# Kernel optimization log

Measured on AMD Instinct MI355X. Metric: run time of the kernel, lower is better.

Reference implementation:

```python
import jax, jax.numpy as jnp
import numpy as np

N_ITER = 2


def _ssn_iter(pixel_features, sh, sw, n_iter=N_ITER):
    """Faithful JAX port of ssn_iter: returns dense abs_affinity (B, ns, N).

    dist[b,k,p] = ||pix[b,:,p] - spix[b,:,cand_k(p)]||^2 over the 3x3 superpixel
    neighborhood of each pixel's initial label; invalid candidates get +inf
    (softmax -> 0), matching the CUDA PairwiseDistFunction + mask semantics.
    """
    B, C, H, W = pixel_features.shape
    nsh, nsw = H // sh, W // sw
    ns = nsh * nsw
    N = H * W

    # calc_init_centroid: adaptive_avg_pool2d == block mean when divisible
    spix = pixel_features.reshape(B, C, nsh, sh, nsw, sw).mean(axis=(3, 5)).reshape(B, C, ns)

    # init_label_map via nearest interpolation == (row//sh)*nsw + col//sw
    r0 = jnp.repeat(jnp.arange(H) // sh, W)            # (N,) superpixel row of each pixel
    c0 = jnp.tile(jnp.arange(W) // sw, H)              # (N,) superpixel col

    # 9 candidate offsets, ordered as [r-nsw, r, r+nsw] with r in [-1,0,1]
    dr = jnp.repeat(jnp.arange(-1, 2), 3)              # (9,)
    dc = jnp.tile(jnp.arange(-1, 2), 3)                # (9,)
    rr = r0[None, :] + dr[:, None]                     # (9, N)
    cc = c0[None, :] + dc[:, None]                     # (9, N)
    valid = (rr >= 0) & (rr < nsh) & (cc >= 0) & (cc < nsw)   # (9, N)
    sidx = jnp.clip(rr * nsw + cc, 0, ns - 1)          # (9, N) candidate superpixel ids
    pidx = jnp.broadcast_to(jnp.arange(N), (9, N))     # (9, N) pixel ids

    pf = pixel_features.reshape(B, C, N)

    def scatter_dense(a):  # a: (9, N) affinity -> dense (ns, N)
        return jnp.zeros((ns, N), a.dtype).at[sidx, pidx].add(a)

    abs_aff = None
    for k in range(n_iter):
        g = spix[:, :, sidx.reshape(-1)].reshape(B, C, 9, N)          # gather candidates
        d = ((pf[:, :, None, :] - g) ** 2).sum(axis=1)                # (B, 9, N)
        d = jnp.where(valid[None], d, jnp.inf)
        aff = jax.nn.softmax(-d, axis=1)                              # invalid -> 0
        aff = jnp.where(valid[None], aff, 0.0)
        abs_aff = jax.vmap(scatter_dense)(aff)                        # (B, ns, N)
        if k < n_iter - 1:
            num = jnp.einsum('bsn,bcn->bsc', abs_aff, pf)             # dense bmm
            den = abs_aff.sum(axis=2)[..., None] + 1e-16
            spix = (num / den).transpose(0, 2, 1)                     # (B, C, ns)
    return abs_aff


def setup_inputs() -> dict:
    key = jax.random.key(0)
    x = jax.random.normal(key, (2, 64, 320, 320), dtype=jnp.float32)
    return {"pixel_features": x, "stoken_h": 16, "stoken_w": 16}


def reference(pixel_features, stoken_h, stoken_w):
    return _ssn_iter(pixel_features, stoken_h, stoken_w, N_ITER)
```

## Files before the change

### kernel.cpp

```cpp
#include <hip/hip_runtime.h>

#define KB   2
#define KC   64
#define KH   320
#define KW   320
#define KSH  16
#define KSW  16
#define KNSH 20
#define KNSW 20
#define KNS  400
#define KN   102400

typedef float float4v __attribute__((ext_vector_type(4)));

__global__ __launch_bounds__(320) void block_mean_kernel(
    const float* __restrict__ pf, float* __restrict__ spix) {
  int wg = blockIdx.x;
  int rb = wg % KNSH;
  int c  = (wg / KNSH) % KC;
  int b  = wg / (KNSH * KC);
  int t  = threadIdx.x;

  const float* row0 = pf + ((size_t)(b * KC + c) * KH + rb * KSH) * KW;
  float acc = 0.f;
#pragma unroll
  for (int i = 0; i < KSH; ++i) acc += row0[i * KW + t];

#pragma unroll
  for (int off = 8; off > 0; off >>= 1) acc += __shfl_down(acc, off, 16);

  if ((t & 15) == 0)
    spix[(b * KC + c) * KNS + rb * KNSW + (t >> 4)] = acc * (1.0f / (KSH * KSW));
}

__global__ __launch_bounds__(256) void dist_partial_kernel(
    const float* __restrict__ pf, const float* __restrict__ spix,
    float* __restrict__ part, float* __restrict__ den) {
  __shared__ float scand[9][KC];
  __shared__ __align__(16) float aff_s[9][256];
  __shared__ float part_s[9][64];
  __shared__ float den_s[9];

  int wg = blockIdx.x;
  int s  = wg % KNS;
  int b  = wg / KNS;
  int sr = s / KNSW, sc = s % KNSW;
  int t  = threadIdx.x;

  for (int idx = t; idx < 9 * KC; idx += 256) {
    int k = idx >> 6, c = idx & 63;
    int rr = sr + k / 3 - 1, cc = sc + k % 3 - 1;
    float v = 0.f;
    if (rr >= 0 && rr < KNSH && cc >= 0 && cc < KNSW)
      v = spix[(b * KC + c) * KNS + rr * KNSW + cc];
    scand[k][c] = v;
  }
  __syncthreads();

  int ti = t >> 4, tj = t & 15;
  int p = (sr * KSH + ti) * KW + sc * KSW + tj;
  const float* pfp = pf + (size_t)b * KC * KN + p;

  float d[9];
#pragma unroll
  for (int k = 0; k < 9; ++k) d[k] = 0.f;
  for (int c = 0; c < KC; ++c) {
    float x = pfp[(size_t)c * KN];
#pragma unroll
    for (int k = 0; k < 9; ++k) {
      float df = x - scand[k][c];
      d[k] = fmaf(df, df, d[k]);
    }
  }
  float m = 3.4e38f;
#pragma unroll
  for (int k = 0; k < 9; ++k) {
    int rr = sr + k / 3 - 1, cc = sc + k % 3 - 1;
    if (rr >= 0 && rr < KNSH && cc >= 0 && cc < KNSW) m = fminf(m, d[k]);
  }
  float e[9];
  float sum = 0.f;
#pragma unroll
  for (int k = 0; k < 9; ++k) {
    int rr = sr + k / 3 - 1, cc = sc + k % 3 - 1;
    bool valid = (rr >= 0 && rr < KNSH && cc >= 0 && cc < KNSW);
    e[k] = valid ? __expf(m - d[k]) : 0.f;
    sum += e[k];
  }
  float inv = 1.0f / sum;
#pragma unroll
  for (int k = 0; k < 9; ++k) aff_s[k][t] = e[k] * inv;
  __syncthreads();

  int w = t >> 6, l = t & 63;
  int li = l >> 2, lj4 = (l & 3) * 4;
  const float* pfb = pf + ((size_t)b * KC + w * 16) * KN
                   + (sr * KSH + li) * KW + sc * KSW + lj4;

  const float4v a0 = *(const float4v*)(&aff_s[0][l * 4]);
  const float4v a1 = *(const float4v*)(&aff_s[1][l * 4]);
  const float4v a2 = *(const float4v*)(&aff_s[2][l * 4]);
  const float4v a3 = *(const float4v*)(&aff_s[3][l * 4]);
  const float4v a4 = *(const float4v*)(&aff_s[4][l * 4]);
  const float4v a5 = *(const float4v*)(&aff_s[5][l * 4]);
  const float4v a6 = *(const float4v*)(&aff_s[6][l * 4]);
  const float4v a7 = *(const float4v*)(&aff_s[7][l * 4]);
  const float4v a8 = *(const float4v*)(&aff_s[8][l * 4]);

  if (w == 0) {
#define DENK(k, av)                                                       \
    {                                                                     \
      float dv = (av.x + av.y) + (av.z + av.w);                           \
      _Pragma("unroll")                                                   \
      for (int off = 32; off > 0; off >>= 1) dv += __shfl_xor(dv, off, 64); \
      if (l == 0) den_s[k] = dv;                                          \
    }
    DENK(0, a0) DENK(1, a1) DENK(2, a2) DENK(3, a3) DENK(4, a4)
    DENK(5, a5) DENK(6, a6) DENK(7, a7) DENK(8, a8)
#undef DENK
  }

#pragma unroll
  for (int cb = 0; cb < 4; ++cb) {
    float4v x0 = *(const float4v*)(pfb + (size_t)(cb * 4 + 0) * KN);
    float4v x1 = *(const float4v*)(pfb + (size_t)(cb * 4 + 1) * KN);
    float4v x2 = *(const float4v*)(pfb + (size_t)(cb * 4 + 2) * KN);
    float4v x3 = *(const float4v*)(pfb + (size_t)(cb * 4 + 3) * KN);

    float acc[4][9];
#define DOTS(c, xv)                                                        \
    acc[c][0] = fmaf(xv.x, a0.x, fmaf(xv.y, a0.y, fmaf(xv.z, a0.z, xv.w * a0.w))); \
    acc[c][1] = fmaf(xv.x, a1.x, fmaf(xv.y, a1.y, fmaf(xv.z, a1.z, xv.w * a1.w))); \
    acc[c][2] = fmaf(xv.x, a2.x, fmaf(xv.y, a2.y, fmaf(xv.z, a2.z, xv.w * a2.w))); \
    acc[c][3] = fmaf(xv.x, a3.x, fmaf(xv.y, a3.y, fmaf(xv.z, a3.z, xv.w * a3.w))); \
    acc[c][4] = fmaf(xv.x, a4.x, fmaf(xv.y, a4.y, fmaf(xv.z, a4.z, xv.w * a4.w))); \
    acc[c][5] = fmaf(xv.x, a5.x, fmaf(xv.y, a5.y, fmaf(xv.z, a5.z, xv.w * a5.w))); \
    acc[c][6] = fmaf(xv.x, a6.x, fmaf(xv.y, a6.y, fmaf(xv.z, a6.z, xv.w * a6.w))); \
    acc[c][7] = fmaf(xv.x, a7.x, fmaf(xv.y, a7.y, fmaf(xv.z, a7.z, xv.w * a7.w))); \
    acc[c][8] = fmaf(xv.x, a8.x, fmaf(xv.y, a8.y, fmaf(xv.z, a8.z, xv.w * a8.w)));
    DOTS(0, x0) DOTS(1, x1) DOTS(2, x2) DOTS(3, x3)
#undef DOTS

#pragma unroll
    for (int off = 32; off > 0; off >>= 1)
#pragma unroll
      for (int c = 0; c < 4; ++c)
#pragma unroll
        for (int k = 0; k < 9; ++k)
          acc[c][k] += __shfl_xor(acc[c][k], off, 64);

    if (l == 0) {
#pragma unroll
      for (int c = 0; c < 4; ++c)
#pragma unroll
        for (int k = 0; k < 9; ++k)
          part_s[k][w * 16 + cb * 4 + c] = acc[c][k];
    }
  }
  __syncthreads();

  size_t base = ((size_t)b * KNS + s) * 9;
  for (int idx = t; idx < 9 * 64; idx += 256)
    part[base * 64 + idx] = part_s[idx >> 6][idx & 63];
  if (t < 9) den[base + t] = den_s[t];
}

__global__ __launch_bounds__(256) void dist_aff2_kernel(
    const float* __restrict__ pf, const float* __restrict__ part,
    const float* __restrict__ den, float* __restrict__ aff) {
  __shared__ float scand[9][KC];

  int wg = blockIdx.x;
  int s  = wg % KNS;
  int b  = wg / KNS;
  int sr = s / KNSW, sc = s % KNSW;
  int t  = threadIdx.x;

  for (int idx = t; idx < 9 * KC; idx += 256) {
    int k = idx >> 6, c = idx & 63;
    int nr = sr + k / 3 - 1, nc = sc + k % 3 - 1;
    float v = 0.f;
    if (nr >= 0 && nr < KNSH && nc >= 0 && nc < KNSW) {
      float num = 0.f, dsum = 0.f;
#pragma unroll
      for (int j = 0; j < 9; ++j) {
        int rr = nr + j / 3 - 1, cc = nc + j % 3 - 1;
        if (rr >= 0 && rr < KNSH && cc >= 0 && cc < KNSW) {
          size_t base = ((size_t)b * KNS + rr * KNSW + cc) * 9 + (8 - j);
          num  += part[base * 64 + c];
          dsum += den[base];
        }
      }
      v = num / (dsum + 1e-16f);
    }
    scand[k][c] = v;
  }
  __syncthreads();

  int i = t >> 4, j = t & 15;
  int p = (sr * KSH + i) * KW + sc * KSW + j;
  const float* pfb = pf + (size_t)b * KC * KN + p;

  float d[9];
#pragma unroll
  for (int k = 0; k < 9; ++k) d[k] = 0.f;

  for (int c = 0; c < KC; ++c) {
    float x = pfb[(size_t)c * KN];
#pragma unroll
    for (int k = 0; k < 9; ++k) {
      float df = x - scand[k][c];
      d[k] = fmaf(df, df, d[k]);
    }
  }

  float m = 3.4e38f;
#pragma unroll
  for (int k = 0; k < 9; ++k) {
    int rr = sr + k / 3 - 1, cc = sc + k % 3 - 1;
    bool valid = (rr >= 0 && rr < KNSH && cc >= 0 && cc < KNSW);
    if (valid) m = fminf(m, d[k]);
  }
  float e[9];
  float sum = 0.f;
#pragma unroll
  for (int k = 0; k < 9; ++k) {
    int rr = sr + k / 3 - 1, cc = sc + k % 3 - 1;
    bool valid = (rr >= 0 && rr < KNSH && cc >= 0 && cc < KNSW);
    e[k] = valid ? __expf(m - d[k]) : 0.f;
    sum += e[k];
  }
  float inv = 1.0f / sum;
#pragma unroll
  for (int k = 0; k < 9; ++k)
    aff[((size_t)b * 9 + k) * KN + p] = e[k] * inv;
}

__global__ __launch_bounds__(256) void write_out_kernel(
    const float* __restrict__ aff, float* __restrict__ out) {
  int wg = blockIdx.x;
  int s  = wg % KNS;
  int b  = wg / KNS;
  int sr = s / KNSW, sc = s % KNSW;
  int t  = threadIdx.x;

  float4v* orow = (float4v*)(out + ((size_t)b * KNS + s) * KN);
  const float* affb = aff + (size_t)b * 9 * KN;

  int it0 = blockIdx.y * 25;
#pragma unroll 5
  for (int ii = 0; ii < 25; ++ii) {
    int q = (it0 + ii) * 256 + t;
    int p = q * 4;
    unsigned r   = (unsigned)p / KW;
    unsigned col = (unsigned)p - r * KW;
    int r0 = (int)(r >> 4), c0 = (int)(col >> 4);
    int dr = sr - r0, dc = sc - c0;
    float4v v = (float4v)(0.f);
    if (dr >= -1 && dr <= 1 && dc >= -1 && dc <= 1) {
      int k = (dr + 1) * 3 + (dc + 1);
      v = *(const float4v*)(affb + (size_t)k * KN + p);
    }
    __builtin_nontemporal_store(v, &orow[q]);
  }
}

extern "C" void kernel_launch(void* const* d_in, const int* in_sizes, int n_in,
                              void* d_out, int out_size, void* d_ws, size_t ws_size,
                              hipStream_t stream) {
  const float* pf = (const float*)d_in[0];
  float* out = (float*)d_out;

  float* spix0 = (float*)d_ws;
  float* affws = spix0 + (size_t)KB * KC * KNS;
  float* partw = affws + (size_t)KB * 9 * KN;
  float* denw  = partw + (size_t)KB * KNS * 9 * 64;

  block_mean_kernel<<<KB * KC * KNSH, 320, 0, stream>>>(pf, spix0);
  dist_partial_kernel<<<KB * KNS, 256, 0, stream>>>(pf, spix0, partw, denw);
  dist_aff2_kernel<<<KB * KNS, 256, 0, stream>>>(pf, partw, denw, affws);
  dim3 gridD(KB * KNS, 4);
  write_out_kernel<<<gridD, 256, 0, stream>>>(affws, out);
}
```

Before: 163.2 us.

## Overlap output zero-fill with compute kernels and write only nonzero tiles

The dense (B, ns, N) output is now zeroed by extra workgroups appended to the two distance kernels, so the zero stores overlap with the compute work. The final kernel then writes only the 3x3 superpixel neighbourhood (48x48 pixels) for each superpixel row instead of scanning the full row. The aim is to hide the large memory-bound zero-fill behind compute and cut the per-element branch logic. The cost is that compute blocks now share bandwidth with the fill, and correctness relies on the sparse writes landing after the zero stores, which holds because of stream ordering.

```diff
diff --git a/kernel.cpp b/kernel.cpp
--- a/kernel.cpp
+++ b/kernel.cpp
@@ -11,7 +11,23 @@
 #define KNS  400
 #define KN   102400
 
+#define TOTF4  20480000L
+#define HALF4  10240000L
+#define NCOMP  800
+#define NZWG   1248
+
 typedef float float4v __attribute__((ext_vector_type(4)));
+
+__device__ __forceinline__ bool zero_duty(float* out, long zstart, long zend) {
+  if (blockIdx.x < NCOMP) return false;
+  long tid = (long)(blockIdx.x - NCOMP) * 256 + threadIdx.x;
+  const long stride = (long)NZWG * 256;
+  float4v z = (float4v)(0.f);
+  float4v* o = (float4v*)out;
+  for (long i = zstart + tid; i < zend; i += stride)
+    __builtin_nontemporal_store(z, &o[i]);
+  return true;
+}
 
 __global__ __launch_bounds__(320) void block_mean_kernel(
     const float* __restrict__ pf, float* __restrict__ spix) {
@@ -35,7 +51,10 @@
 
 __global__ __launch_bounds__(256) void dist_partial_kernel(
     const float* __restrict__ pf, const float* __restrict__ spix,
-    float* __restrict__ part, float* __restrict__ den) {
+    float* __restrict__ part, float* __restrict__ den,
+    float* __restrict__ outz) {
+  if (zero_duty(outz, 0L, HALF4)) return;
+
   __shared__ float scand[9][KC];
   __shared__ __align__(16) float aff_s[9][256];
   __shared__ float part_s[9][64];
@@ -167,7 +186,10 @@
 
 __global__ __launch_bounds__(256) void dist_aff2_kernel(
     const float* __restrict__ pf, const float* __restrict__ part,
-    const float* __restrict__ den, float* __restrict__ aff) {
+    const float* __restrict__ den, float* __restrict__ aff,
+    float* __restrict__ outz) {
+  if (zero_duty(outz, HALF4, TOTF4)) return;
+
   __shared__ float scand[9][KC];
 
   int wg = blockIdx.x;
@@ -236,7 +258,7 @@
     aff[((size_t)b * 9 + k) * KN + p] = e[k] * inv;
 }
 
-__global__ __launch_bounds__(256) void write_out_kernel(
+__global__ __launch_bounds__(256) void sparse_out_kernel(
     const float* __restrict__ aff, float* __restrict__ out) {
   int wg = blockIdx.x;
   int s  = wg % KNS;
@@ -244,24 +266,24 @@
   int sr = s / KNSW, sc = s % KNSW;
   int t  = threadIdx.x;
 
-  float4v* orow = (float4v*)(out + ((size_t)b * KNS + s) * KN);
+  float* orow = out + ((size_t)b * KNS + s) * KN;
   const float* affb = aff + (size_t)b * 9 * KN;
 
-  int it0 = blockIdx.y * 25;
-#pragma unroll 5
-  for (int ii = 0; ii < 25; ++ii) {
-    int q = (it0 + ii) * 256 + t;
-    int p = q * 4;
-    unsigned r   = (unsigned)p / KW;
-    unsigned col = (unsigned)p - r * KW;
-    int r0 = (int)(r >> 4), c0 = (int)(col >> 4);
-    int dr = sr - r0, dc = sc - c0;
-    float4v v = (float4v)(0.f);
-    if (dr >= -1 && dr <= 1 && dc >= -1 && dc <= 1) {
-      int k = (dr + 1) * 3 + (dc + 1);
-      v = *(const float4v*)(affb + (size_t)k * KN + p);
-    }
-    __builtin_nontemporal_store(v, &orow[q]);
+  int rbase  = (sr - 1) * KSH;
+  int c4base = (sc - 1) * 4;
+
+#pragma unroll
+  for (int ii = 0; ii < 3; ++ii) {
+    int idx = ii * 256 + t;
+    if (idx >= 576) break;
+    int vr = idx / 12, vc = idx - vr * 12;
+    int r  = rbase + vr;
+    int c4 = c4base + vc;
+    if (r < 0 || r >= KH || c4 < 0 || c4 >= KW / 4) continue;
+    int k = 8 - (vr >> 4) * 3 - (vc >> 2);
+    int p = r * KW + c4 * 4;
+    float4v v = *(const float4v*)(affb + (size_t)k * KN + p);
+    __builtin_nontemporal_store(v, (float4v*)(orow + p));
   }
 }
 
@@ -277,8 +299,7 @@
   float* denw  = partw + (size_t)KB * KNS * 9 * 64;
 
   block_mean_kernel<<<KB * KC * KNSH, 320, 0, stream>>>(pf, spix0);
-  dist_partial_kernel<<<KB * KNS, 256, 0, stream>>>(pf, spix0, partw, denw);
-  dist_aff2_kernel<<<KB * KNS, 256, 0, stream>>>(pf, partw, denw, affws);
-  dim3 gridD(KB * KNS, 4);
-  write_out_kernel<<<gridD, 256, 0, stream>>>(affws, out);
-}
+  dist_partial_kernel<<<NCOMP + NZWG, 256, 0, stream>>>(pf, spix0, partw, denw, out);
+  dist_aff2_kernel<<<NCOMP + NZWG, 256, 0, stream>>>(pf, partw, denw, affws, out);
+  sparse_out_kernel<<<KB * KNS, 256, 0, stream>>>(affws, out);
+}
```

After: 136.0 us. 16.7% less time.

## Fuse output zero-fill into compute kernels and scatter affinities directly

Applied to the files above, without the earlier changes.

Removes the separate write-out kernel and the affinity workspace. Zero-filling of the dense output is split into three regions handled by extra blocks prepended to each of the three kernels, so the large store traffic overlaps with the compute phases. The final kernel writes softmax affinities directly into the 3x3 band of the output, and its zero blocks skip band positions. The trade-off is less coalesced scalar band stores and fixed split constants that assume the exact problem size.

```diff
diff --git a/kernel.cpp b/kernel.cpp
--- a/kernel.cpp
+++ b/kernel.cpp
@@ -11,11 +11,30 @@
 #define KNS  400
 #define KN   102400
 
+#define TOTF4  20480000u
+#define Z1     6800000u
+#define Z2     13640000u
+#define NZA    1024
+#define NZB    1248
+#define NZC    1248
+#define NCOMPA 2560
+#define NCOMP  800
+
 typedef float float4v __attribute__((ext_vector_type(4)));
 
 __global__ __launch_bounds__(320) void block_mean_kernel(
-    const float* __restrict__ pf, float* __restrict__ spix) {
-  int wg = blockIdx.x;
+    const float* __restrict__ pf, float* __restrict__ spix,
+    float* __restrict__ outz) {
+  if (blockIdx.x < NZA) {
+    unsigned tid = blockIdx.x * 320u + threadIdx.x;
+    const unsigned stride = NZA * 320u;
+    float4v z = (float4v)(0.f);
+    float4v* o = (float4v*)outz;
+    for (unsigned i = tid; i < Z1; i += stride)
+      __builtin_nontemporal_store(z, &o[i]);
+    return;
+  }
+  int wg = blockIdx.x - NZA;
   int rb = wg % KNSH;
   int c  = (wg / KNSH) % KC;
   int b  = wg / (KNSH * KC);
@@ -35,13 +54,24 @@
 
 __global__ __launch_bounds__(256) void dist_partial_kernel(
     const float* __restrict__ pf, const float* __restrict__ spix,
-    float* __restrict__ part, float* __restrict__ den) {
+    float* __restrict__ part, float* __restrict__ den,
+    float* __restrict__ outz) {
+  if (blockIdx.x < NZB) {
+    unsigned tid = blockIdx.x * 256u + threadIdx.x;
+    const unsigned stride = NZB * 256u;
+    float4v z = (float4v)(0.f);
+    float4v* o = (float4v*)outz;
+    for (unsigned i = Z1 + tid; i < Z2; i += stride)
+      __builtin_nontemporal_store(z, &o[i]);
+    return;
+  }
+
   __shared__ float scand[9][KC];
   __shared__ __align__(16) float aff_s[9][256];
   __shared__ float part_s[9][64];
   __shared__ float den_s[9];
 
-  int wg = blockIdx.x;
+  int wg = blockIdx.x - NZB;
   int s  = wg % KNS;
   int b  = wg / KNS;
   int sr = s / KNSW, sc = s % KNSW;
@@ -165,12 +195,32 @@
   if (t < 9) den[base + t] = den_s[t];
 }
 
-__global__ __launch_bounds__(256) void dist_aff2_kernel(
+__global__ __launch_bounds__(256) void dist_band_kernel(
     const float* __restrict__ pf, const float* __restrict__ part,
-    const float* __restrict__ den, float* __restrict__ aff) {
+    const float* __restrict__ den, float* __restrict__ out) {
+  if (blockIdx.x < NZC) {
+    unsigned tid = blockIdx.x * 256u + threadIdx.x;
+    const unsigned stride = NZC * 256u;
+    float4v z = (float4v)(0.f);
+    float4v* o = (float4v*)out;
+    for (unsigned i = Z2 + tid; i < TOTF4; i += stride) {
+      unsigned orow = i / 25600u;
+      unsigned f4   = i - orow * 25600u;
+      unsigned s    = orow % KNS;
+      unsigned p    = f4 * 4u;
+      int sr = (int)(s / KNSW), sc = (int)(s % KNSW);
+      int r0 = (int)(p / 5120u);
+      int c0 = (int)((p % KW) >> 4);
+      int dr = sr - r0, dc = sc - c0;
+      if (dr < -1 || dr > 1 || dc < -1 || dc > 1)
+        __builtin_nontemporal_store(z, &o[i]);
+    }
+    return;
+  }
+
   __shared__ float scand[9][KC];
 
-  int wg = blockIdx.x;
+  int wg = blockIdx.x - NZC;
   int s  = wg % KNS;
   int b  = wg / KNS;
   int sr = s / KNSW, sc = s % KNSW;
@@ -231,37 +281,13 @@
     sum += e[k];
   }
   float inv = 1.0f / sum;
-#pragma unroll
-  for (int k = 0; k < 9; ++k)
-    aff[((size_t)b * 9 + k) * KN + p] = e[k] * inv;
-}
-
-__global__ __launch_bounds__(256) void write_out_kernel(
-    const float* __restrict__ aff, float* __restrict__ out) {
-  int wg = blockIdx.x;
-  int s  = wg % KNS;
-  int b  = wg / KNS;
-  int sr = s / KNSW, sc = s % KNSW;
-  int t  = threadIdx.x;
-
-  float4v* orow = (float4v*)(out + ((size_t)b * KNS + s) * KN);
-  const float* affb = aff + (size_t)b * 9 * KN;
-
-  int it0 = blockIdx.y * 25;
-#pragma unroll 5
-  for (int ii = 0; ii < 25; ++ii) {
-    int q = (it0 + ii) * 256 + t;
-    int p = q * 4;
-    unsigned r   = (unsigned)p / KW;
-    unsigned col = (unsigned)p - r * KW;
-    int r0 = (int)(r >> 4), c0 = (int)(col >> 4);
-    int dr = sr - r0, dc = sc - c0;
-    float4v v = (float4v)(0.f);
-    if (dr >= -1 && dr <= 1 && dc >= -1 && dc <= 1) {
-      int k = (dr + 1) * 3 + (dc + 1);
-      v = *(const float4v*)(affb + (size_t)k * KN + p);
-    }
-    __builtin_nontemporal_store(v, &orow[q]);
+
+#pragma unroll
+  for (int k = 0; k < 9; ++k) {
+    int rr = sr + k / 3 - 1, cc = sc + k % 3 - 1;
+    if (rr >= 0 && rr < KNSH && cc >= 0 && cc < KNSW)
+      __builtin_nontemporal_store(e[k] * inv,
+          out + ((size_t)b * KNS + rr * KNSW + cc) * KN + p);
   }
 }
 
@@ -272,13 +298,10 @@
   float* out = (float*)d_out;
 
   float* spix0 = (float*)d_ws;
-  float* affws = spix0 + (size_t)KB * KC * KNS;
-  float* partw = affws + (size_t)KB * 9 * KN;
+  float* partw = spix0 + (size_t)KB * KC * KNS;
   float* denw  = partw + (size_t)KB * KNS * 9 * 64;
 
-  block_mean_kernel<<<KB * KC * KNSH, 320, 0, stream>>>(pf, spix0);
-  dist_partial_kernel<<<KB * KNS, 256, 0, stream>>>(pf, spix0, partw, denw);
-  dist_aff2_kernel<<<KB * KNS, 256, 0, stream>>>(pf, partw, denw, affws);
-  dim3 gridD(KB * KNS, 4);
-  write_out_kernel<<<gridD, 256, 0, stream>>>(affws, out);
+  block_mean_kernel<<<NZA + NCOMPA, 320, 0, stream>>>(pf, spix0, out);
+  dist_partial_kernel<<<NZB + NCOMP, 256, 0, stream>>>(pf, spix0, partw, denw, out);
+  dist_band_kernel<<<NZC + NCOMP, 256, 0, stream>>>(pf, partw, denw, out);
 }
```

After: 144.9 us. 11.2% less time.
